# Kernel tuning notes

Hardware: AMD Instinct MI355X
Metric: run time of the kernel (lower is better)

The kernel has to match this reference:

```python
import jax, jax.numpy as jnp
import numpy as np

N, K, D = 131072, 1024, 128
COMMITMENT_COST = 0.25


def setup_inputs() -> dict:
    key = jax.random.key(0)
    k1, k2 = jax.random.split(key)
    c_input = jax.random.normal(k1, (N, D), dtype=jnp.float32)
    # nn.Embedding weight initialized N(0, 0.1)
    embedding_weight = jax.random.normal(k2, (K, D), dtype=jnp.float32) * 0.1
    return {"c_input": c_input, "embedding_weight": embedding_weight}


def reference(c_input, embedding_weight):
    distances = (
        jnp.sum(c_input ** 2, axis=1, keepdims=True)
        + jnp.sum(embedding_weight ** 2, axis=1)
        - 2.0 * jnp.matmul(c_input, embedding_weight.T)
    )
    encoding_indices = jnp.argmin(distances, axis=1)  # [N]
    encodings = jax.nn.one_hot(encoding_indices, K, dtype=c_input.dtype)  # [N, K]
    # one-hot @ weight == direct gather
    quantized = embedding_weight[encoding_indices]  # [N, D]
    e_latent_loss = jnp.mean((jax.lax.stop_gradient(quantized) - c_input) ** 2)
    q_latent_loss = jnp.mean((quantized - jax.lax.stop_gradient(c_input)) ** 2)
    loss = q_latent_loss + COMMITMENT_COST * e_latent_loss
    # straight-through estimator
    quantized_st = c_input + jax.lax.stop_gradient(quantized - c_input)
    return (loss, quantized_st, encodings)
```

## Files before the change

kernel.cpp:

```cpp
#include <hip/hip_runtime.h>
#include <hip/hip_bf16.h>

#define NROWS 131072
#define KC 1024
#define DD 128
#define MARGIN 1e-3f

typedef __attribute__((ext_vector_type(8))) short short8;
typedef __attribute__((ext_vector_type(4))) float f32x4;

__device__ inline short f2bf_hi(float f) {
  unsigned u = __builtin_bit_cast(unsigned, f);
  u += 0x7fffu + ((u >> 16) & 1u);
  return (short)(u >> 16);
}
__device__ inline float bf2f(short s) {
  unsigned u = ((unsigned)(unsigned short)s) << 16;
  return __builtin_bit_cast(float, u);
}

__global__ void vq_prep(const float* __restrict__ E, short* __restrict__ EH,
                        short* __restrict__ EL, float* __restrict__ SE,
                        float* __restrict__ out) {
  int b = blockIdx.x, t = threadIdx.x;
  if (b < 64) {
    int idx = b * 256 + t;
    int s = (idx >> 6) & 3, l = idx & 63;
    int c = idx >> 8;
    int q = l >> 4, n = l & 15;
    const float* src = E + (16 * c + n) * DD + 32 * s + 8 * q;
    short8 h, lo;
#pragma unroll
    for (int j = 0; j < 8; ++j) {
      float x = src[j];
      short hb = f2bf_hi(x);
      h[j] = hb;
      lo[j] = f2bf_hi(x - bf2f(hb));
    }
    *(short8*)(EH + idx * 8) = h;
    *(short8*)(EL + idx * 8) = lo;
  } else {
    if (t == 0) out[0] = 0.f;
    for (int k = t; k < KC; k += 256) {
      double acc = 0.0;
      const float* er = E + k * DD;
      for (int i = 0; i < DD; ++i) { double v = (double)er[i]; acc += v * v; }
      SE[k] = (float)acc;
    }
  }
}

__global__ __launch_bounds__(256, 4) void vq_main(
    const float* __restrict__ X, const float* __restrict__ E,
    const short* __restrict__ EH, const short* __restrict__ EL,
    const float* __restrict__ SE, float* __restrict__ out) {
  __shared__ __align__(16) short lbh[8192];
  __shared__ __align__(16) short lbl[8192];
  __shared__ int lidx[128];
  __shared__ int lflag[128];
  __shared__ int lany;
  __shared__ float lx[128];
  __shared__ float lrv[256];
  __shared__ int lri[256];
  __shared__ float lsx;
  __shared__ float lloss[4];

  const int tid = threadIdx.x;
  const int w = tid >> 6, l = tid & 63, q = l >> 4, n = l & 15;
  const int row_base = blockIdx.x * 128;
  if (tid == 0) lany = 0;

  short8 ah[2][4], al[2][4];
#pragma unroll
  for (int mt = 0; mt < 2; ++mt) {
    const float* xp = X + (row_base + 32 * w + 16 * mt + n) * DD + 8 * q;
#pragma unroll
    for (int s = 0; s < 4; ++s) {
      f32x4 x0 = *(const f32x4*)(xp + 32 * s);
      f32x4 x1 = *(const f32x4*)(xp + 32 * s + 4);
#pragma unroll
      for (int j = 0; j < 4; ++j) {
        short hb = f2bf_hi(x0[j]);
        ah[mt][s][j] = hb;
        al[mt][s][j] = f2bf_hi(x0[j] - bf2f(hb));
        short hb2 = f2bf_hi(x1[j]);
        ah[mt][s][j + 4] = hb2;
        al[mt][s][j + 4] = f2bf_hi(x1[j] - bf2f(hb2));
      }
    }
  }

  float bestv[8], secv[8];
  int besti[8];
#pragma unroll
  for (int i = 0; i < 8; ++i) { bestv[i] = -3e38f; secv[i] = -3e38f; besti[i] = 0; }

  for (int cc = 0; cc < 16; ++cc) {
    {
      const short8* gh = (const short8*)(EH + cc * 8192);
      const short8* gl = (const short8*)(EL + cc * 8192);
      short8* dh = (short8*)lbh;
      short8* dl = (short8*)lbl;
#pragma unroll
      for (int i = 0; i < 4; ++i) {
        int u = i * 256 + tid;
        dh[u] = gh[u];
        dl[u] = gl[u];
      }
    }
    __syncthreads();

    f32x4 acc[2][4];
#pragma unroll
    for (int mt = 0; mt < 2; ++mt)
#pragma unroll
      for (int nt = 0; nt < 4; ++nt) acc[mt][nt] = (f32x4){0.f, 0.f, 0.f, 0.f};

#pragma unroll
    for (int nt = 0; nt < 4; ++nt) {
#pragma unroll
      for (int s = 0; s < 4; ++s) {
        short8 bh  = *(const short8*)(lbh + ((nt * 4 + s) * 64 + l) * 8);
        short8 blo = *(const short8*)(lbl + ((nt * 4 + s) * 64 + l) * 8);
        acc[0][nt] = __builtin_amdgcn_mfma_f32_16x16x32_bf16(ah[0][s], bh,  acc[0][nt], 0, 0, 0);
        acc[1][nt] = __builtin_amdgcn_mfma_f32_16x16x32_bf16(ah[1][s], bh,  acc[1][nt], 0, 0, 0);
        acc[0][nt] = __builtin_amdgcn_mfma_f32_16x16x32_bf16(al[0][s], bh,  acc[0][nt], 0, 0, 0);
        acc[1][nt] = __builtin_amdgcn_mfma_f32_16x16x32_bf16(al[1][s], bh,  acc[1][nt], 0, 0, 0);
        acc[0][nt] = __builtin_amdgcn_mfma_f32_16x16x32_bf16(ah[0][s], blo, acc[0][nt], 0, 0, 0);
        acc[1][nt] = __builtin_amdgcn_mfma_f32_16x16x32_bf16(ah[1][s], blo, acc[1][nt], 0, 0, 0);
      }
    }
    __syncthreads();

#pragma unroll
    for (int nt = 0; nt < 4; ++nt) {
      int k = cc * 64 + nt * 16 + n;
      float hse = 0.5f * SE[k];
#pragma unroll
      for (int mt = 0; mt < 2; ++mt)
#pragma unroll
        for (int r = 0; r < 4; ++r) {
          float sc = acc[mt][nt][r] - hse;
          int slot = mt * 4 + r;
          bool gt = sc > bestv[slot];
          secv[slot] = gt ? bestv[slot] : fmaxf(secv[slot], sc);
          if (gt) { bestv[slot] = sc; besti[slot] = k; }
        }
    }
  }

#pragma unroll
  for (int slot = 0; slot < 8; ++slot) {
    float v = bestv[slot], s2 = secv[slot];
    int bi = besti[slot];
#pragma unroll
    for (int m = 1; m <= 8; m <<= 1) {
      float v2 = __shfl_xor(v, m, 64);
      float sv2 = __shfl_xor(s2, m, 64);
      int i2 = __shfl_xor(bi, m, 64);
      float ns = fmaxf(fminf(v, v2), fmaxf(s2, sv2));
      if (v2 > v || (v2 == v && i2 < bi)) { v = v2; bi = i2; }
      s2 = ns;
    }
    if (n == 0) {
      int mt = slot >> 2, r = slot & 3;
      int rl = 32 * w + 16 * mt + 4 * q + r;
      int f = (v - s2) <= MARGIN;
      lidx[rl] = bi;
      lflag[rl] = f;
      if (f) lany = 1;
    }
  }
  __syncthreads();

  if (lany) {
    for (int rl = 0; rl < 128; ++rl) {
      if (lflag[rl] == 0) continue;
      if (tid < DD) lx[tid] = X[(row_base + rl) * DD + tid];
      __syncthreads();
      if (tid == 0) {
        double sx = 0.0;
        for (int i = 0; i < DD; ++i) { double v = (double)lx[i]; sx += v * v; }
        lsx = (float)sx;
      }
      __syncthreads();
      float dmin = 3e38f; int kmin = 0;
      for (int kk = tid; kk < KC; kk += 256) {
        double dot = 0.0;
        const float* er = E + kk * DD;
        for (int i = 0; i < DD; ++i) dot += (double)lx[i] * (double)er[i];
        float a = lsx + SE[kk];
        float b2 = (float)(2.0 * dot);
        float dnp = a - b2;
        if (dnp < dmin) { dmin = dnp; kmin = kk; }
      }
      lrv[tid] = dmin; lri[tid] = kmin;
      __syncthreads();
      if (tid == 0) {
        float dm = lrv[0]; int km = lri[0];
        for (int t2 = 1; t2 < 256; ++t2)
          if (lrv[t2] < dm || (lrv[t2] == dm && lri[t2] < km)) { dm = lrv[t2]; km = lri[t2]; }
        lidx[rl] = km;
      }
      __syncthreads();
    }
  }
  __syncthreads();

  float lp = 0.f;
  const int encb = 1 + NROWS * DD;
  for (int rl = w; rl < 128; rl += 4) {
    int row = row_base + rl;
    int idx = lidx[rl];
    float x0 = X[row * DD + l];
    float x1 = X[row * DD + 64 + l];
    float e0 = E[idx * DD + l];
    float e1 = E[idx * DD + 64 + l];
    float d0 = e0 - x0, d1 = e1 - x1;
    __builtin_nontemporal_store(x0 + d0, out + 1 + row * DD + l);
    __builtin_nontemporal_store(x1 + d1, out + 1 + row * DD + 64 + l);
    lp += d0 * d0 + d1 * d1;
    if (l == 0) out[encb + row * KC + idx] = 1.0f;
  }
#pragma unroll
  for (int m = 1; m < 64; m <<= 1) lp += __shfl_xor(lp, m, 64);
  if (l == 0) lloss[w] = lp;
  __syncthreads();
  if (tid == 0) {
    float t = (lloss[0] + lloss[1] + lloss[2] + lloss[3]) *
              (1.25f / ((float)NROWS * (float)DD));
    atomicAdd(out, t);
  }
}

extern "C" void kernel_launch(void* const* d_in, const int* in_sizes, int n_in,
                              void* d_out, int out_size, void* d_ws, size_t ws_size,
                              hipStream_t stream) {
  const float* X = (const float*)d_in[0];
  const float* E = (const float*)d_in[1];
  float* out = (float*)d_out;
  short* EH = (short*)d_ws;
  short* EL = EH + KC * DD;
  float* SE = (float*)(EL + KC * DD);
  size_t encb = (size_t)1 + (size_t)NROWS * DD;
  hipMemsetAsync(out + encb, 0, (size_t)NROWS * KC * sizeof(float), stream);
  vq_prep<<<65, 256, 0, stream>>>(E, EH, EL, SE, out);
  vq_main<<<NROWS / 128, 256, 0, stream>>>(X, E, EH, EL, SE, out);
}
```

Before: 908.7 us.

## Write one-hot rows directly in kernel, drop memset, rotate codebook chunks

Result: faster. 832.7 us (-8.4%).

```diff
diff --git a/kernel.cpp b/kernel.cpp
--- a/kernel.cpp
+++ b/kernel.cpp
@@ -56,19 +56,22 @@
     const float* __restrict__ SE, float* __restrict__ out) {
   __shared__ __align__(16) short lbh[8192];
   __shared__ __align__(16) short lbl[8192];
+  __shared__ __align__(16) float lse[KC];
   __shared__ int lidx[128];
   __shared__ int lflag[128];
   __shared__ int lany;
   __shared__ float lx[128];
-  __shared__ float lrv[256];
-  __shared__ int lri[256];
+  __shared__ float lrv[4];
+  __shared__ int lri[4];
   __shared__ float lsx;
   __shared__ float lloss[4];
 
   const int tid = threadIdx.x;
   const int w = tid >> 6, l = tid & 63, q = l >> 4, n = l & 15;
   const int row_base = blockIdx.x * 128;
+  const int rot = blockIdx.x & 15;
   if (tid == 0) lany = 0;
+  *(f32x4*)(lse + tid * 4) = *(const f32x4*)(SE + tid * 4);
 
   short8 ah[2][4], al[2][4];
 #pragma unroll
@@ -96,9 +99,10 @@
   for (int i = 0; i < 8; ++i) { bestv[i] = -3e38f; secv[i] = -3e38f; besti[i] = 0; }
 
   for (int cc = 0; cc < 16; ++cc) {
+    const int ccr = (cc + rot) & 15;
     {
-      const short8* gh = (const short8*)(EH + cc * 8192);
-      const short8* gl = (const short8*)(EL + cc * 8192);
+      const short8* gh = (const short8*)(EH + ccr * 8192);
+      const short8* gl = (const short8*)(EL + ccr * 8192);
       short8* dh = (short8*)lbh;
       short8* dl = (short8*)lbl;
 #pragma unroll
@@ -134,8 +138,8 @@
 
 #pragma unroll
     for (int nt = 0; nt < 4; ++nt) {
-      int k = cc * 64 + nt * 16 + n;
-      float hse = 0.5f * SE[k];
+      int k = ccr * 64 + nt * 16 + n;
+      float hse = 0.5f * lse[k];
 #pragma unroll
       for (int mt = 0; mt < 2; ++mt)
 #pragma unroll
@@ -178,10 +182,12 @@
       if (lflag[rl] == 0) continue;
       if (tid < DD) lx[tid] = X[(row_base + rl) * DD + tid];
       __syncthreads();
-      if (tid == 0) {
-        double sx = 0.0;
-        for (int i = 0; i < DD; ++i) { double v = (double)lx[i]; sx += v * v; }
-        lsx = (float)sx;
+      if (tid < 64) {
+        double v0 = lx[tid], v1 = lx[tid + 64];
+        double s = v0 * v0 + v1 * v1;
+#pragma unroll
+        for (int m = 1; m < 64; m <<= 1) s += __shfl_xor(s, m, 64);
+        if (tid == 0) lsx = (float)s;
       }
       __syncthreads();
       float dmin = 3e38f; int kmin = 0;
@@ -189,16 +195,23 @@
         double dot = 0.0;
         const float* er = E + kk * DD;
         for (int i = 0; i < DD; ++i) dot += (double)lx[i] * (double)er[i];
-        float a = lsx + SE[kk];
+        float a = lsx + lse[kk];
         float b2 = (float)(2.0 * dot);
         float dnp = a - b2;
         if (dnp < dmin) { dmin = dnp; kmin = kk; }
       }
-      lrv[tid] = dmin; lri[tid] = kmin;
+#pragma unroll
+      for (int m = 1; m < 64; m <<= 1) {
+        float v2 = __shfl_xor(dmin, m, 64);
+        int k2 = __shfl_xor(kmin, m, 64);
+        if (v2 < dmin || (v2 == dmin && k2 < kmin)) { dmin = v2; kmin = k2; }
+      }
+      if (l == 0) { lrv[w] = dmin; lri[w] = kmin; }
       __syncthreads();
       if (tid == 0) {
         float dm = lrv[0]; int km = lri[0];
-        for (int t2 = 1; t2 < 256; ++t2)
+#pragma unroll
+        for (int t2 = 1; t2 < 4; ++t2)
           if (lrv[t2] < dm || (lrv[t2] == dm && lri[t2] < km)) { dm = lrv[t2]; km = lri[t2]; }
         lidx[rl] = km;
       }
@@ -220,7 +233,18 @@
     __builtin_nontemporal_store(x0 + d0, out + 1 + row * DD + l);
     __builtin_nontemporal_store(x1 + d1, out + 1 + row * DD + 64 + l);
     lp += d0 * d0 + d1 * d1;
-    if (l == 0) out[encb + row * KC + idx] = 1.0f;
+    float* ob = out + encb + row * KC;
+    if (l < 3) __builtin_nontemporal_store((l == idx) ? 1.f : 0.f, ob + l);
+    for (int c = l; c < 255; c += 64) {
+      int eb = 3 + 4 * c;
+      f32x4 v;
+      v[0] = (eb     == idx) ? 1.f : 0.f;
+      v[1] = (eb + 1 == idx) ? 1.f : 0.f;
+      v[2] = (eb + 2 == idx) ? 1.f : 0.f;
+      v[3] = (eb + 3 == idx) ? 1.f : 0.f;
+      __builtin_nontemporal_store(v, (f32x4*)(ob + eb));
+    }
+    if (l == 63) __builtin_nontemporal_store((1023 == idx) ? 1.f : 0.f, ob + 1023);
   }
 #pragma unroll
   for (int m = 1; m < 64; m <<= 1) lp += __shfl_xor(lp, m, 64);
@@ -242,8 +266,6 @@
   short* EH = (short*)d_ws;
   short* EL = EH + KC * DD;
   float* SE = (float*)(EL + KC * DD);
-  size_t encb = (size_t)1 + (size_t)NROWS * DD;
-  hipMemsetAsync(out + encb, 0, (size_t)NROWS * KC * sizeof(float), stream);
   vq_prep<<<65, 256, 0, stream>>>(E, EH, EL, SE, out);
   vq_main<<<NROWS / 128, 256, 0, stream>>>(X, E, EH, EL, SE, out);
 }
```
